# Kernel optimization log

Measured on AMD Instinct MI355X. Metric: run time of the kernel, lower is better.

Reference implementation:

```python
import jax, jax.numpy as jnp
import numpy as np

THETA = 10000.0

def _rope(x, cos, sin):
    # x: [B, S, D]; cos/sin: [S, D/2]. Pairs are (x[..., 2i], x[..., 2i+1]) treated as complex.
    xr = x.reshape(*x.shape[:-1], -1, 2)
    x0, x1 = xr[..., 0], xr[..., 1]
    o0 = x0 * cos - x1 * sin
    o1 = x0 * sin + x1 * cos
    return jnp.stack([o0, o1], axis=-1).reshape(x.shape)

def setup_inputs() -> dict:
    key = jax.random.key(0)
    ks = jax.random.split(key, 7)
    B, S, D = 4, 2048, 1024
    sd = 1.0 / np.sqrt(D)
    return {
        "x": jax.random.normal(ks[0], (B, S, D), dtype=jnp.float32),
        "wq_w": jax.random.normal(ks[1], (D, D), dtype=jnp.float32) * sd,
        "wq_b": jax.random.normal(ks[2], (D,), dtype=jnp.float32) * 0.01,
        "wk_w": jax.random.normal(ks[3], (D, D), dtype=jnp.float32) * sd,
        "wk_b": jax.random.normal(ks[4], (D,), dtype=jnp.float32) * 0.01,
        "wv_w": jax.random.normal(ks[5], (D, D), dtype=jnp.float32) * sd,
        "wv_b": jax.random.normal(ks[6], (D,), dtype=jnp.float32) * 0.01,
    }

def reference(x, wq_w, wq_b, wk_w, wk_b, wv_w, wv_b):
    B, S, D = x.shape
    # QKV projections (torch Linear: y = x @ W.T + b)
    q = jnp.einsum('bsd,ed->bse', x, wq_w) + wq_b
    k = jnp.einsum('bsd,ed->bse', x, wk_w) + wk_b
    v = jnp.einsum('bsd,ed->bse', x, wv_w) + wv_b
    # Rotary embedding: freqs_cis[t, i] = exp(i * t / theta^(2i/D))
    inv_freq = 1.0 / (THETA ** (jnp.arange(0, D, 2, dtype=jnp.float32) / D))  # [D/2]
    ang = jnp.arange(S, dtype=jnp.float32)[:, None] * inv_freq[None, :]  # [S, D/2]
    cos, sin = jnp.cos(ang), jnp.sin(ang)
    q = _rope(q, cos, sin)
    k = _rope(k, cos, sin)
    # Full (non-causal, single-head) attention with scale 1/sqrt(dim)
    scores = jnp.einsum('bqd,bkd->bqk', q, k) / jnp.sqrt(jnp.float32(D))
    probs = jax.nn.softmax(scores.astype(jnp.float32), axis=-1)
    return jnp.einsum('bqk,bkd->bqd', probs, v)
```

## Files before the change

kernel.cpp:

```cpp
#include <hip/hip_runtime.h>
#include <cstdint>

using u16 = unsigned short;
using u32 = unsigned int;

typedef __attribute__((ext_vector_type(8))) short short8;
typedef __attribute__((ext_vector_type(4))) float floatx4;

__device__ __forceinline__ u16 f2bf(float f) {
    u32 u = __float_as_uint(f);
    u32 r = u + 0x7fffu + ((u >> 16) & 1u);
    return (u16)(r >> 16);
}
__device__ __forceinline__ float bf2f(u16 h) {
    return __uint_as_float(((u32)h) << 16);
}

__global__ void cvt_f32_to_bf16(const float* __restrict__ in, u16* __restrict__ out, long n) {
    long i = ((long)blockIdx.x * blockDim.x + threadIdx.x) * 4;
    if (i >= n) return;
    float4 v = *reinterpret_cast<const float4*>(in + i);
    uint2 o;
    o.x = (u32)f2bf(v.x) | ((u32)f2bf(v.y) << 16);
    o.y = (u32)f2bf(v.z) | ((u32)f2bf(v.w) << 16);
    *reinterpret_cast<uint2*>(out + i) = o;
}

__global__ void cvt3(const float* __restrict__ w0, const float* __restrict__ w1,
                     const float* __restrict__ w2,
                     u16* __restrict__ o0, u16* __restrict__ o1, u16* __restrict__ o2,
                     const float* __restrict__ qb, const float* __restrict__ kb,
                     float* __restrict__ bqk) {
    int b = blockIdx.x;
    if (b >= 3072) {
        int i = (b - 3072) * 256 + threadIdx.x;
        bqk[i] = (i < 1024) ? qb[i] : kb[i - 1024];
        return;
    }
    int seg = b >> 10;
    const float* src; u16* dst;
    if (seg == 0)      { src = w0; dst = o0; }
    else if (seg == 1) { src = w1; dst = o1; }
    else               { src = w2; dst = o2; }
    long i = ((long)(b & 1023) * 256 + threadIdx.x) * 4;
    float4 v = *reinterpret_cast<const float4*>(src + i);
    uint2 o;
    o.x = (u32)f2bf(v.x) | ((u32)f2bf(v.y) << 16);
    o.y = (u32)f2bf(v.z) | ((u32)f2bf(v.w) << 16);
    *reinterpret_cast<uint2*>(dst + i) = o;
}

__device__ __forceinline__ void async_cp16(const u16* g, u16* l) {
    __builtin_amdgcn_global_load_lds(
        (const __attribute__((address_space(1))) void*)g,
        (__attribute__((address_space(3))) void*)l, 16, 0, 0);
}

template <bool BF16_OUT>
__device__ __forceinline__ void gemm_core(
    const u16* __restrict__ A, const u16* __restrict__ B, void* __restrict__ Cv,
    int K, int lda, int ldb, int ldc,
    long tile_m, long tile_n, long cbase,
    const float* bias_col, const float* bias_row,
    float scale, bool rope, u16* smem)
{
    u16* As = smem;
    u16* Bs = smem + 8192;

    const int tid  = threadIdx.x;
    const int lane = tid & 63;
    const int wave = tid >> 6;
    const int wm = (wave >> 1) << 6;
    const int wn = (wave & 1) << 6;

    floatx4 acc[4][4] = {};

    const int srow = tid >> 2;
    const int skp  = (((tid & 3) ^ (srow & 3))) * 8;
    const u16* Ag = A + (tile_m + srow) * (long)lda + skp;
    const u16* Bg = B + (tile_n + srow) * (long)ldb + skp;
    u16* Asl = &As[tid * 8];
    u16* Bsl = &Bs[tid * 8];

    const int fm  = lane & 15;
    const int fks = (((lane >> 4) ^ (lane & 3))) * 8;

    for (int k0 = 0; k0 < K; k0 += 64) {
        async_cp16(Ag,                       Asl);
        async_cp16(Ag + 64 * (long)lda,      Asl + 64 * 32);
        async_cp16(Ag + 32,                  Asl + 4096);
        async_cp16(Ag + 32 + 64 * (long)lda, Asl + 4096 + 64 * 32);
        async_cp16(Bg,                       Bsl);
        async_cp16(Bg + 64 * (long)ldb,      Bsl + 64 * 32);
        async_cp16(Bg + 32,                  Bsl + 4096);
        async_cp16(Bg + 32 + 64 * (long)ldb, Bsl + 4096 + 64 * 32);
        Ag += 64; Bg += 64;
        __syncthreads();

        #pragma unroll
        for (int c = 0; c < 2; ++c) {
            const u16* Ap = As + c * 4096;
            const u16* Bp = Bs + c * 4096;
            short8 af[4], bfr[4];
            #pragma unroll
            for (int i = 0; i < 4; ++i)
                af[i] = *reinterpret_cast<const short8*>(&Ap[(wm + i * 16 + fm) * 32 + fks]);
            #pragma unroll
            for (int j = 0; j < 4; ++j)
                bfr[j] = *reinterpret_cast<const short8*>(&Bp[(wn + j * 16 + fm) * 32 + fks]);
            #pragma unroll
            for (int i = 0; i < 4; ++i)
                #pragma unroll
                for (int j = 0; j < 4; ++j)
                    acc[i][j] = __builtin_amdgcn_mfma_f32_16x16x32_bf16(af[i], bfr[j], acc[i][j], 0, 0, 0);
        }
        __syncthreads();
    }

    const int q4  = lane >> 4;
    const int c16 = lane & 15;
    float* smemf  = (float*)smem;
    float* myeps = smemf + wave * (16 * 68);
    const long n0 = tile_n + wn + c16 * 4;

    float4 bc4 = make_float4(0.f, 0.f, 0.f, 0.f);
    if (bias_col) bc4 = *reinterpret_cast<const float4*>(bias_col + n0);

    float inv0 = 0.f, inv1 = 0.f;
    if (rope) {
        int p0 = (int)(n0 >> 1);
        inv0 = __expf((float)(p0 & 511)       * -1.79889463e-2f);
        inv1 = __expf((float)((p0 + 1) & 511) * -1.79889463e-2f);
    }

    #pragma unroll
    for (int i = 0; i < 4; ++i) {
        __syncthreads();
        #pragma unroll
        for (int j = 0; j < 4; ++j)
            #pragma unroll
            for (int r = 0; r < 4; ++r)
                myeps[(q4 * 4 + r) * 68 + j * 16 + c16] = acc[i][j][r];
        __syncthreads();
        #pragma unroll
        for (int p = 0; p < 4; ++p) {
            int lrow = p * 4 + q4;
            long m = tile_m + wm + i * 16 + lrow;
            float4 v = *reinterpret_cast<const float4*>(&myeps[lrow * 68 + c16 * 4]);
            v.x = v.x * scale + bc4.x;
            v.y = v.y * scale + bc4.y;
            v.z = v.z * scale + bc4.z;
            v.w = v.w * scale + bc4.w;
            if (bias_row) {
                float br = bias_row[m];
                v.x += br; v.y += br; v.z += br; v.w += br;
            }
            if (rope) {
                int s = (int)(m & 2047);
                float a0 = (float)s * inv0, a1 = (float)s * inv1;
                float sn0 = __sinf(a0), cs0 = __cosf(a0);
                float sn1 = __sinf(a1), cs1 = __cosf(a1);
                float x0 = v.x, x1 = v.y, x2 = v.z, x3 = v.w;
                v.x = x0 * cs0 - x1 * sn0;
                v.y = x0 * sn0 + x1 * cs0;
                v.z = x2 * cs1 - x3 * sn1;
                v.w = x2 * sn1 + x3 * cs1;
            }
            long off = cbase + m * (long)ldc + n0;
            if constexpr (BF16_OUT) {
                uint2 o;
                o.x = (u32)f2bf(v.x) | ((u32)f2bf(v.y) << 16);
                o.y = (u32)f2bf(v.z) | ((u32)f2bf(v.w) << 16);
                *reinterpret_cast<uint2*>((u16*)Cv + off) = o;
            } else {
                *reinterpret_cast<float4*>((float*)Cv + off) = v;
            }
        }
    }
}

template <bool BF16_OUT>
__global__ __launch_bounds__(256)
void gemm_nt(const u16* __restrict__ A, const u16* __restrict__ B, void* __restrict__ Cv,
             int K, int lda, int ldb, int ldc,
             long sA, long sB, long sC,
             const float* __restrict__ bias_col, const float* __restrict__ bias_row,
             float scale)
{
    const u32 gx = gridDim.x, gy = gridDim.y;
    u32 id = blockIdx.x + gx * (blockIdx.y + gy * blockIdx.z);
    const u32 G = gx * gy * gridDim.z;
    if ((G & 7u) == 0u) id = (id & 7u) * (G >> 3) + (id >> 3);
    const u32 bx = id % gx;
    const u32 t1 = id / gx;
    const u32 by = t1 % gy;
    const u32 bz = t1 / gy;

    __shared__ alignas(16) u16 smem[16384];
    gemm_core<BF16_OUT>(A + (long)bz * sA, B + (long)bz * sB, Cv,
                        K, lda, ldb, ldc,
                        (long)by * 128, (long)bx * 128, (long)bz * sC,
                        bias_col, bias_row, scale, false, smem);
}

__global__ __launch_bounds__(256)
void gemm_fused12(const u16* __restrict__ xb, const u16* __restrict__ wqk,
                  const u16* __restrict__ wv, u16* __restrict__ QK, u16* __restrict__ VT,
                  const float* __restrict__ bqk, const float* __restrict__ wvb)
{
    u32 id = blockIdx.x;
    id = (id & 7u) * 192u + (id >> 3);
    __shared__ alignas(16) u16 smem[16384];
    if (id < 1024u) {
        u32 bx = id & 15u, by = id >> 4;
        gemm_core<true>(xb, wqk, QK, 1024, 1024, 1024, 2048,
                        (long)by * 128, (long)bx * 128, 0L,
                        bqk, nullptr, 1.0f, true, smem);
    } else {
        u32 r = id - 1024u;
        u32 bx = r & 15u, by = (r >> 4) & 7u, bz = r >> 7;
        gemm_core<true>(wv, xb + (long)bz * 2048 * 1024, VT,
                        1024, 1024, 1024, 2048,
                        (long)by * 128, (long)bx * 128, (long)bz * 1024 * 2048,
                        nullptr, wvb, 1.0f, false, smem);
    }
}

__global__ __launch_bounds__(256)
void softmax_kernel(const u16* __restrict__ S, u16* __restrict__ P) {
    long row = blockIdx.x;
    const u16* s = S + row * 2048;
    u16* p = P + row * 2048;
    int tid = threadIdx.x;
    uint4 raw = *reinterpret_cast<const uint4*>(s + tid * 8);
    float v[8];
    v[0] = bf2f((u16)(raw.x & 0xffffu)); v[1] = bf2f((u16)(raw.x >> 16));
    v[2] = bf2f((u16)(raw.y & 0xffffu)); v[3] = bf2f((u16)(raw.y >> 16));
    v[4] = bf2f((u16)(raw.z & 0xffffu)); v[5] = bf2f((u16)(raw.z >> 16));
    v[6] = bf2f((u16)(raw.w & 0xffffu)); v[7] = bf2f((u16)(raw.w >> 16));
    float mx = v[0];
    #pragma unroll
    for (int j = 1; j < 8; ++j) mx = fmaxf(mx, v[j]);
    #pragma unroll
    for (int off = 32; off; off >>= 1) mx = fmaxf(mx, __shfl_xor(mx, off));
    __shared__ float redm[4];
    __shared__ float reds[4];
    int lane = tid & 63, wv = tid >> 6;
    if (lane == 0) redm[wv] = mx;
    __syncthreads();
    mx = fmaxf(fmaxf(redm[0], redm[1]), fmaxf(redm[2], redm[3]));
    float sum = 0.0f;
    #pragma unroll
    for (int j = 0; j < 8; ++j) { v[j] = __expf(v[j] - mx); sum += v[j]; }
    #pragma unroll
    for (int off = 32; off; off >>= 1) sum += __shfl_xor(sum, off);
    if (lane == 0) reds[wv] = sum;
    __syncthreads();
    sum = reds[0] + reds[1] + reds[2] + reds[3];
    float inv = 1.0f / sum;
    uint4 o;
    o.x = (u32)f2bf(v[0] * inv) | ((u32)f2bf(v[1] * inv) << 16);
    o.y = (u32)f2bf(v[2] * inv) | ((u32)f2bf(v[3] * inv) << 16);
    o.z = (u32)f2bf(v[4] * inv) | ((u32)f2bf(v[5] * inv) << 16);
    o.w = (u32)f2bf(v[6] * inv) | ((u32)f2bf(v[7] * inv) << 16);
    *reinterpret_cast<uint4*>(&p[tid * 8]) = o;
}

extern "C" void kernel_launch(void* const* d_in, const int* in_sizes, int n_in,
                              void* d_out, int out_size, void* d_ws, size_t ws_size,
                              hipStream_t stream)
{
    const float* x   = (const float*)d_in[0];
    const float* wqw = (const float*)d_in[1];
    const float* wqb = (const float*)d_in[2];
    const float* wkw = (const float*)d_in[3];
    const float* wkb = (const float*)d_in[4];
    const float* wvw = (const float*)d_in[5];
    const float* wvb = (const float*)d_in[6];
    float* out = (float*)d_out;

    char* ws = (char*)d_ws;
    const size_t MB = 1ull << 20;
    u16*   Sbuf = (u16*)(ws + 0);
    u16*   Pbuf = (u16*)(ws + 64 * MB);
    u16*   QK   = (u16*)(ws + 96 * MB);
    u16*   VT   = (u16*)(ws + 128 * MB);
    u16*   xb    = (u16*)(ws + 0);
    u16*   wqk   = (u16*)(ws + 16 * MB);
    u16*   wvbuf = (u16*)(ws + 20 * MB);
    float* bqk   = (float*)(ws + 22 * MB);

    cvt_f32_to_bf16<<<dim3(8192), 256, 0, stream>>>(x, xb, 8192L * 1024);
    cvt3<<<dim3(3080), 256, 0, stream>>>(wqw, wkw, wvw, wqk, wqk + 1024 * 1024, wvbuf,
                                         wqb, wkb, bqk);

    gemm_fused12<<<dim3(1536), 256, 0, stream>>>(xb, wqk, wvbuf, QK, VT, bqk, wvb);

    gemm_nt<true><<<dim3(16, 16, 4), 256, 0, stream>>>(
        QK, QK + 1024, Sbuf, 1024, 2048, 2048, 2048,
        2048L * 2048, 2048L * 2048, 2048L * 2048, nullptr, nullptr, 0.03125f);

    softmax_kernel<<<dim3(8192), 256, 0, stream>>>(Sbuf, Pbuf);

    gemm_nt<false><<<dim3(8, 16, 4), 256, 0, stream>>>(
        Pbuf, VT, out, 2048, 2048, 2048, 1024,
        2048L * 2048, 1024L * 2048, 2048L * 1024, nullptr, nullptr, 1.0f);

    (void)in_sizes; (void)n_in; (void)out_size; (void)ws_size;
}
```

Baseline: 272.8 us.

## Shrink GEMM LDS tiles, stagger K start per block, add N=64 PV GEMM

Merges the x and weight conversion kernels into one launch. The main GEMM core moves from a K-step of 64 to 32, halving shared memory so more blocks can be resident per CU. Each block now starts its K loop at a phase offset derived from its block id, spreading concurrent blocks across different K slices of the operands. The final P·V GEMM uses a new 128x64-tile kernel with twice as many blocks to fill the device better. The cost is more barriers per unit of work and smaller MFMA batches between syncs.

```diff
diff --git a/kernel.cpp b/kernel.cpp
--- a/kernel.cpp
+++ b/kernel.cpp
@@ -16,33 +16,29 @@
     return __uint_as_float(((u32)h) << 16);
 }
 
-__global__ void cvt_f32_to_bf16(const float* __restrict__ in, u16* __restrict__ out, long n) {
-    long i = ((long)blockIdx.x * blockDim.x + threadIdx.x) * 4;
-    if (i >= n) return;
-    float4 v = *reinterpret_cast<const float4*>(in + i);
-    uint2 o;
-    o.x = (u32)f2bf(v.x) | ((u32)f2bf(v.y) << 16);
-    o.y = (u32)f2bf(v.z) | ((u32)f2bf(v.w) << 16);
-    *reinterpret_cast<uint2*>(out + i) = o;
-}
-
-__global__ void cvt3(const float* __restrict__ w0, const float* __restrict__ w1,
-                     const float* __restrict__ w2,
-                     u16* __restrict__ o0, u16* __restrict__ o1, u16* __restrict__ o2,
-                     const float* __restrict__ qb, const float* __restrict__ kb,
-                     float* __restrict__ bqk) {
+__global__ void cvt_all(const float* __restrict__ x, u16* __restrict__ xb,
+                        const float* __restrict__ w0, const float* __restrict__ w1,
+                        const float* __restrict__ w2,
+                        u16* __restrict__ o0, u16* __restrict__ o1, u16* __restrict__ o2,
+                        const float* __restrict__ qb, const float* __restrict__ kb,
+                        float* __restrict__ bqk)
+{
     int b = blockIdx.x;
-    if (b >= 3072) {
-        int i = (b - 3072) * 256 + threadIdx.x;
+    if (b >= 11264) {
+        int i = (b - 11264) * 256 + threadIdx.x;
         bqk[i] = (i < 1024) ? qb[i] : kb[i - 1024];
         return;
     }
-    int seg = b >> 10;
-    const float* src; u16* dst;
-    if (seg == 0)      { src = w0; dst = o0; }
-    else if (seg == 1) { src = w1; dst = o1; }
-    else               { src = w2; dst = o2; }
-    long i = ((long)(b & 1023) * 256 + threadIdx.x) * 4;
+    const float* src; u16* dst; long base;
+    if (b < 8192) { src = x; dst = xb; base = (long)b; }
+    else {
+        int r = b - 8192, seg = r >> 10;
+        if (seg == 0)      { src = w0; dst = o0; }
+        else if (seg == 1) { src = w1; dst = o1; }
+        else               { src = w2; dst = o2; }
+        base = (long)(r & 1023);
+    }
+    long i = (base * 256 + threadIdx.x) * 4;
     float4 v = *reinterpret_cast<const float4*>(src + i);
     uint2 o;
     o.x = (u32)f2bf(v.x) | ((u32)f2bf(v.y) << 16);
@@ -62,10 +58,10 @@
     int K, int lda, int ldb, int ldc,
     long tile_m, long tile_n, long cbase,
     const float* bias_col, const float* bias_row,
-    float scale, bool rope, u16* smem)
+    float scale, bool rope, int phase0, u16* smem)
 {
     u16* As = smem;
-    u16* Bs = smem + 8192;
+    u16* Bs = smem + 4096;
 
     const int tid  = threadIdx.x;
     const int lane = tid & 63;
@@ -77,49 +73,43 @@
 
     const int srow = tid >> 2;
     const int skp  = (((tid & 3) ^ (srow & 3))) * 8;
-    const u16* Ag = A + (tile_m + srow) * (long)lda + skp;
-    const u16* Bg = B + (tile_n + srow) * (long)ldb + skp;
+    const u16* Agb = A + (tile_m + srow) * (long)lda + skp;
+    const u16* Bgb = B + (tile_n + srow) * (long)ldb + skp;
     u16* Asl = &As[tid * 8];
     u16* Bsl = &Bs[tid * 8];
 
     const int fm  = lane & 15;
     const int fks = (((lane >> 4) ^ (lane & 3))) * 8;
 
-    for (int k0 = 0; k0 < K; k0 += 64) {
-        async_cp16(Ag,                       Asl);
-        async_cp16(Ag + 64 * (long)lda,      Asl + 64 * 32);
-        async_cp16(Ag + 32,                  Asl + 4096);
-        async_cp16(Ag + 32 + 64 * (long)lda, Asl + 4096 + 64 * 32);
-        async_cp16(Bg,                       Bsl);
-        async_cp16(Bg + 64 * (long)ldb,      Bsl + 64 * 32);
-        async_cp16(Bg + 32,                  Bsl + 4096);
-        async_cp16(Bg + 32 + 64 * (long)ldb, Bsl + 4096 + 64 * 32);
-        Ag += 64; Bg += 64;
-        __syncthreads();
-
-        #pragma unroll
-        for (int c = 0; c < 2; ++c) {
-            const u16* Ap = As + c * 4096;
-            const u16* Bp = Bs + c * 4096;
-            short8 af[4], bfr[4];
-            #pragma unroll
-            for (int i = 0; i < 4; ++i)
-                af[i] = *reinterpret_cast<const short8*>(&Ap[(wm + i * 16 + fm) * 32 + fks]);
+    const int nIter = K >> 5;
+    int kki = phase0;
+    for (int it = 0; it < nIter; ++it) {
+        const int kk = kki << 5;
+        async_cp16(Agb + kk,                  Asl);
+        async_cp16(Agb + kk + 64 * (long)lda, Asl + 64 * 32);
+        async_cp16(Bgb + kk,                  Bsl);
+        async_cp16(Bgb + kk + 64 * (long)ldb, Bsl + 64 * 32);
+        if (++kki == nIter) kki = 0;
+        __syncthreads();
+
+        short8 af[4], bfr[4];
+        #pragma unroll
+        for (int i = 0; i < 4; ++i)
+            af[i] = *reinterpret_cast<const short8*>(&As[(wm + i * 16 + fm) * 32 + fks]);
+        #pragma unroll
+        for (int j = 0; j < 4; ++j)
+            bfr[j] = *reinterpret_cast<const short8*>(&Bs[(wn + j * 16 + fm) * 32 + fks]);
+        #pragma unroll
+        for (int i = 0; i < 4; ++i)
             #pragma unroll
             for (int j = 0; j < 4; ++j)
-                bfr[j] = *reinterpret_cast<const short8*>(&Bp[(wn + j * 16 + fm) * 32 + fks]);
-            #pragma unroll
-            for (int i = 0; i < 4; ++i)
-                #pragma unroll
-                for (int j = 0; j < 4; ++j)
-                    acc[i][j] = __builtin_amdgcn_mfma_f32_16x16x32_bf16(af[i], bfr[j], acc[i][j], 0, 0, 0);
-        }
+                acc[i][j] = __builtin_amdgcn_mfma_f32_16x16x32_bf16(af[i], bfr[j], acc[i][j], 0, 0, 0);
         __syncthreads();
     }
 
     const int q4  = lane >> 4;
     const int c16 = lane & 15;
-    float* smemf  = (float*)smem;
+    float* smemf = (float*)smem;
     float* myeps = smemf + wave * (16 * 68);
     const long n0 = tile_n + wn + c16 * 4;
 
@@ -135,7 +125,6 @@
 
     #pragma unroll
     for (int i = 0; i < 4; ++i) {
-        __syncthreads();
         #pragma unroll
         for (int j = 0; j < 4; ++j)
             #pragma unroll
@@ -176,6 +165,100 @@
                 *reinterpret_cast<float4*>((float*)Cv + off) = v;
             }
         }
+        __syncthreads();
+    }
+}
+
+template <bool BF16_OUT>
+__device__ __forceinline__ void gemm_core_n64(
+    const u16* __restrict__ A, const u16* __restrict__ B, void* __restrict__ Cv,
+    int K, int lda, int ldb, int ldc,
+    long tile_m, long tile_n, long cbase,
+    float scale, int phase0, u16* smem)
+{
+    u16* As = smem;
+    u16* Bs = smem + 8192;
+
+    const int tid  = threadIdx.x;
+    const int lane = tid & 63;
+    const int wave = tid >> 6;
+    const int wm = (wave >> 1) << 6;
+    const int wn = (wave & 1) << 5;
+
+    floatx4 acc[4][2] = {};
+
+    const int srow = tid >> 2;
+    const int skp  = (((tid & 3) ^ (srow & 3))) * 8;
+    const u16* Agb = A + (tile_m + srow) * (long)lda + skp;
+    const u16* Bgb = B + (tile_n + srow) * (long)ldb + skp;
+    u16* Asl = &As[tid * 8];
+    u16* Bsl = &Bs[tid * 8];
+
+    const int fm  = lane & 15;
+    const int fks = (((lane >> 4) ^ (lane & 3))) * 8;
+
+    const int nIter = K >> 6;
+    int kki = phase0;
+    for (int it = 0; it < nIter; ++it) {
+        const int kk = kki << 6;
+        async_cp16(Agb + kk,                       Asl);
+        async_cp16(Agb + kk + 64 * (long)lda,      Asl + 64 * 32);
+        async_cp16(Agb + kk + 32,                  Asl + 4096);
+        async_cp16(Agb + kk + 32 + 64 * (long)lda, Asl + 4096 + 64 * 32);
+        async_cp16(Bgb + kk,                       Bsl);
+        async_cp16(Bgb + kk + 32,                  Bsl + 2048);
+        if (++kki == nIter) kki = 0;
+        __syncthreads();
+
+        #pragma unroll
+        for (int c = 0; c < 2; ++c) {
+            const u16* Ap = As + c * 4096;
+            const u16* Bp = Bs + c * 2048;
+            short8 af[4], bfr[2];
+            #pragma unroll
+            for (int i = 0; i < 4; ++i)
+                af[i] = *reinterpret_cast<const short8*>(&Ap[(wm + i * 16 + fm) * 32 + fks]);
+            #pragma unroll
+            for (int j = 0; j < 2; ++j)
+                bfr[j] = *reinterpret_cast<const short8*>(&Bp[(wn + j * 16 + fm) * 32 + fks]);
+            #pragma unroll
+            for (int i = 0; i < 4; ++i)
+                #pragma unroll
+                for (int j = 0; j < 2; ++j)
+                    acc[i][j] = __builtin_amdgcn_mfma_f32_16x16x32_bf16(af[i], bfr[j], acc[i][j], 0, 0, 0);
+        }
+        __syncthreads();
+    }
+
+    const int q4  = lane >> 4;
+    const int c16 = lane & 15;
+    float* smemf = (float*)smem;
+    float* myeps = smemf + wave * (16 * 36);
+    const long n0 = tile_n + wn + c16 * 2;
+
+    #pragma unroll
+    for (int i = 0; i < 4; ++i) {
+        #pragma unroll
+        for (int j = 0; j < 2; ++j)
+            #pragma unroll
+            for (int r = 0; r < 4; ++r)
+                myeps[(q4 * 4 + r) * 36 + j * 16 + c16] = acc[i][j][r];
+        __syncthreads();
+        #pragma unroll
+        for (int p = 0; p < 4; ++p) {
+            int lrow = p * 4 + q4;
+            long m = tile_m + wm + i * 16 + lrow;
+            float2 v = *reinterpret_cast<const float2*>(&myeps[lrow * 36 + c16 * 2]);
+            v.x *= scale; v.y *= scale;
+            long off = cbase + m * (long)ldc + n0;
+            if constexpr (BF16_OUT) {
+                *reinterpret_cast<u32*>((u16*)Cv + off) =
+                    (u32)f2bf(v.x) | ((u32)f2bf(v.y) << 16);
+            } else {
+                *reinterpret_cast<float2*>((float*)Cv + off) = v;
+            }
+        }
+        __syncthreads();
     }
 }
 
@@ -196,11 +279,34 @@
     const u32 by = t1 % gy;
     const u32 bz = t1 / gy;
 
-    __shared__ alignas(16) u16 smem[16384];
+    __shared__ alignas(16) u16 smem[8704];
     gemm_core<BF16_OUT>(A + (long)bz * sA, B + (long)bz * sB, Cv,
                         K, lda, ldb, ldc,
                         (long)by * 128, (long)bx * 128, (long)bz * sC,
-                        bias_col, bias_row, scale, false, smem);
+                        bias_col, bias_row, scale, false,
+                        (int)(id & (u32)((K >> 5) - 1)), smem);
+}
+
+template <bool BF16_OUT>
+__global__ __launch_bounds__(256)
+void gemm_nt_n64(const u16* __restrict__ A, const u16* __restrict__ B, void* __restrict__ Cv,
+                 int K, int lda, int ldb, int ldc,
+                 long sA, long sB, long sC, float scale)
+{
+    const u32 gx = gridDim.x, gy = gridDim.y;
+    u32 id = blockIdx.x + gx * (blockIdx.y + gy * blockIdx.z);
+    const u32 G = gx * gy * gridDim.z;
+    if ((G & 7u) == 0u) id = (id & 7u) * (G >> 3) + (id >> 3);
+    const u32 bx = id % gx;
+    const u32 t1 = id / gx;
+    const u32 by = t1 % gy;
+    const u32 bz = t1 / gy;
+
+    __shared__ alignas(16) u16 smem[12288];
+    gemm_core_n64<BF16_OUT>(A + (long)bz * sA, B + (long)bz * sB, Cv,
+                            K, lda, ldb, ldc,
+                            (long)by * 128, (long)bx * 64, (long)bz * sC,
+                            scale, (int)(id & (u32)((K >> 6) - 1)), smem);
 }
 
 __global__ __launch_bounds__(256)
@@ -210,19 +316,19 @@
 {
     u32 id = blockIdx.x;
     id = (id & 7u) * 192u + (id >> 3);
-    __shared__ alignas(16) u16 smem[16384];
+    __shared__ alignas(16) u16 smem[8704];
     if (id < 1024u) {
         u32 bx = id & 15u, by = id >> 4;
         gemm_core<true>(xb, wqk, QK, 1024, 1024, 1024, 2048,
                         (long)by * 128, (long)bx * 128, 0L,
-                        bqk, nullptr, 1.0f, true, smem);
+                        bqk, nullptr, 1.0f, true, (int)(id & 31u), smem);
     } else {
         u32 r = id - 1024u;
         u32 bx = r & 15u, by = (r >> 4) & 7u, bz = r >> 7;
         gemm_core<true>(wv, xb + (long)bz * 2048 * 1024, VT,
                         1024, 1024, 1024, 2048,
                         (long)by * 128, (long)bx * 128, (long)bz * 1024 * 2048,
-                        nullptr, wvb, 1.0f, false, smem);
+                        nullptr, wvb, 1.0f, false, (int)(r & 31u), smem);
     }
 }
 
@@ -290,9 +396,9 @@
     u16*   wvbuf = (u16*)(ws + 20 * MB);
     float* bqk   = (float*)(ws + 22 * MB);
 
-    cvt_f32_to_bf16<<<dim3(8192), 256, 0, stream>>>(x, xb, 8192L * 1024);
-    cvt3<<<dim3(3080), 256, 0, stream>>>(wqw, wkw, wvw, wqk, wqk + 1024 * 1024, wvbuf,
-                                         wqb, wkb, bqk);
+    cvt_all<<<dim3(11272), 256, 0, stream>>>(x, xb, wqw, wkw, wvw,
+                                             wqk, wqk + 1024 * 1024, wvbuf,
+                                             wqb, wkb, bqk);
 
     gemm_fused12<<<dim3(1536), 256, 0, stream>>>(xb, wqk, wvbuf, QK, VT, bqk, wvb);
 
@@ -302,9 +408,9 @@
 
     softmax_kernel<<<dim3(8192), 256, 0, stream>>>(Sbuf, Pbuf);
 
-    gemm_nt<false><<<dim3(8, 16, 4), 256, 0, stream>>>(
+    gemm_nt_n64<false><<<dim3(16, 16, 4), 256, 0, stream>>>(
         Pbuf, VT, out, 2048, 2048, 2048, 1024,
-        2048L * 2048, 1024L * 2048, 2048L * 1024, nullptr, nullptr, 1.0f);
+        2048L * 2048, 1024L * 2048, 2048L * 1024, 1.0f);
 
     (void)in_sizes; (void)n_in; (void)out_size; (void)ws_size;
 }
```

New measurement: 317.8 us. 1.16x slower.
